# Kernel tuning notes

Measured on AMD Instinct MI355X. Metric: run time of the kernel, lower is better.

The kernel has to match this reference:

```python
import jax, jax.numpy as jnp
import numpy as np

N, E, D_IN, H, L, G = 50000, 800000, 128, 64, 3, 256
EPS_BN = 1e-5


def setup_inputs() -> dict:
    key = jax.random.key(0)
    ks = jax.random.split(key, 8)
    x = jax.random.normal(ks[0], (N, D_IN), dtype=jnp.float32)
    edge_index = jax.random.randint(ks[1], (2, E), 0, N)
    batch = jnp.sort(jax.random.randint(ks[2], (N,), 0, G))
    dims = [D_IN] + [H] * L
    params = {}
    for l in range(L):
        params[f"W{l}"] = jax.random.normal(ks[3 + l], (dims[l], H), jnp.float32) * (1.0 / np.sqrt(dims[l]))
        params[f"b{l}"] = jnp.zeros((H,), jnp.float32)
        params[f"gamma{l}"] = jnp.ones((H,), jnp.float32)
        params[f"beta{l}"] = jnp.zeros((H,), jnp.float32)
    return {"x": x, "edge_index": edge_index, "batch": batch, **params}


def _gcn_forward(x, edge_index, batch, Ws, bs, gammas, betas):
    n = x.shape[0]
    loop = jnp.arange(n)
    # GCNConv adds self-loops, then symmetric D^{-1/2} (A+I) D^{-1/2} normalization
    src = jnp.concatenate([edge_index[0], loop])
    dst = jnp.concatenate([edge_index[1], loop])
    deg = jax.ops.segment_sum(jnp.ones_like(src, jnp.float32), dst, num_segments=n)
    dinv = jax.lax.rsqrt(jnp.maximum(deg, 1.0))  # deg >= 1 thanks to self-loops
    norm = dinv[src] * dinv[dst]  # [E+N]

    zs = []
    z = x
    for W, b, g, be in zip(Ws, bs, gammas, betas):
        h = z @ W  # transform first, then aggregate (PyG GCNConv)
        agg = jax.ops.segment_sum(h[src] * norm[:, None], dst, num_segments=n) + b
        z = jax.nn.relu(agg)
        mu = z.mean(axis=0)
        var = z.var(axis=0)  # biased, as in BatchNorm training mode
        z = (z - mu) * jax.lax.rsqrt(var + EPS_BN) * g + be
        zs.append(z)

    cnt = jnp.maximum(
        jax.ops.segment_sum(jnp.ones((n,), jnp.float32), batch, num_segments=G), 1.0
    )
    gs = [jax.ops.segment_sum(z_, batch, num_segments=G) / cnt[:, None] for z_ in zs]

    zc = jnp.concatenate(zs, axis=1)  # [N, L*H]
    gc = jnp.concatenate(gs, axis=1)  # [G, L*H]

    def l2n(a):
        return a / jnp.maximum(jnp.linalg.norm(a, axis=1, keepdims=True), 1e-12)

    return l2n(zc), l2n(gc)


def reference(x, edge_index, batch, W0, b0, gamma0, beta0, W1, b1, gamma1, beta1, W2, b2, gamma2, beta2):
    return _gcn_forward(
        x, edge_index, batch,
        [W0, W1, W2], [b0, b1, b2],
        [gamma0, gamma1, gamma2], [beta0, beta1, beta2],
    )
```

## Files before the change

### kernel.cpp

```cpp
#include <hip/hip_runtime.h>
#include <hip/hip_fp16.h>
#include <cstdint>
#include <cstddef>

#define N_NODES 50000
#define N_EDGES 800000
#define DIM_IN 128
#define H_DIM 64
#define N_GRAPHS 256
#define EPS_BN 1e-5f
#define GEMM0_BLOCKS 782
#define CBLK 128
#define CHUNK 6250
#define HWORDS4 6250
#define SMEM_WORDS (DIM_IN * 64)

struct __align__(16) h8 { __half2 a, b, c, d; };
struct __align__(8)  h4 { __half2 a, b; };

__device__ inline void fma4(float4& a, float s, const float4& w) {
    a.x = fmaf(s, w.x, a.x);
    a.y = fmaf(s, w.y, a.y);
    a.z = fmaf(s, w.z, a.z);
    a.w = fmaf(s, w.w, a.w);
}

__device__ inline h4 pack_h4(float4 v) {
    h4 r;
    r.a = __float22half2_rn(make_float2(v.x, v.y));
    r.b = __float22half2_rn(make_float2(v.z, v.w));
    return r;
}


__global__ __launch_bounds__(256) void count_hist_k(const int* __restrict__ dst,
                                                    unsigned char* __restrict__ histG) {
    __shared__ unsigned int h[HWORDS4];
    for (int i = threadIdx.x; i < HWORDS4; i += 256) h[i] = 0;
    __syncthreads();
    int base = blockIdx.x * CHUNK;
    for (int i = threadIdx.x; i < CHUNK; i += 256) {
        int n = dst[base + i];
        atomicAdd(&h[n >> 3], 1u << (4 * (n & 7)));
    }
    __syncthreads();
    unsigned char* out = histG + (size_t)blockIdx.x * N_NODES;
    for (int n = threadIdx.x; n < N_NODES; n += 256)
        out[n] = (h[n >> 3] >> (4 * (n & 7))) & 0xF;
}

__global__ void blockscan_k(const unsigned char* __restrict__ histG,
                            unsigned char* __restrict__ baseG, int* __restrict__ counts) {
    int n = blockIdx.x * 256 + threadIdx.x;
    if (n >= N_NODES) return;
    int tot = 0;
    for (int b = 0; b < CBLK; b++) {
        unsigned char v = histG[(size_t)b * N_NODES + n];
        baseG[(size_t)b * N_NODES + n] = (unsigned char)tot;
        tot += v;
    }
    counts[n] = tot;
}

__global__ void scan_block_k(const int* __restrict__ counts, int* __restrict__ offsets,
                             int* __restrict__ blocksums) {
    __shared__ int sh[1024];
    int i = blockIdx.x * 1024 + threadIdx.x;
    int v = (i < N_NODES) ? counts[i] : 0;
    sh[threadIdx.x] = v;
    __syncthreads();
    for (int off = 1; off < 1024; off <<= 1) {
        int t = (threadIdx.x >= off) ? sh[threadIdx.x - off] : 0;
        __syncthreads();
        sh[threadIdx.x] += t;
        __syncthreads();
    }
    if (i < N_NODES) offsets[i] = sh[threadIdx.x] - v;
    if (threadIdx.x == 1023) blocksums[blockIdx.x] = sh[1023];
}

__global__ void scan_sums_k(int* blocksums, int nb) {
    if (threadIdx.x == 0 && blockIdx.x == 0) {
        int run = 0;
        for (int b = 0; b < nb; b++) { int t = blocksums[b]; blocksums[b] = run; run += t; }
    }
}

__global__ void finalize_offsets_k(int* __restrict__ offsets,
                                   const int* __restrict__ counts,
                                   const int* __restrict__ blocksums,
                                   float* __restrict__ dinv) {
    int i = blockIdx.x * blockDim.x + threadIdx.x;
    if (i >= N_NODES) return;
    offsets[i] = offsets[i] + blocksums[i >> 10];
    dinv[i] = rsqrtf((float)(counts[i] + 1));
}


__global__ __launch_bounds__(256) void gemm0_fill_k(
        const float* __restrict__ X, const float* __restrict__ W,
        const float* __restrict__ dinv, __half* __restrict__ hp,
        const int* __restrict__ src, const int* __restrict__ dst,
        const int* __restrict__ offsets, const unsigned char* __restrict__ baseG,
        unsigned short* __restrict__ ssrc) {
    __shared__ __align__(16) unsigned int smem[SMEM_WORDS];
    if (blockIdx.x < CBLK) {
        int b = blockIdx.x;
        for (int i = threadIdx.x; i < HWORDS4; i += 256) smem[i] = 0;
        __syncthreads();
        int base = b * CHUNK;
        const unsigned char* myBase = baseG + (size_t)b * N_NODES;
        for (int i = threadIdx.x; i < CHUNK; i += 256) {
            int n = dst[base + i];
            int s = src[base + i];
            unsigned int old = atomicAdd(&smem[n >> 3], 1u << (4 * (n & 7)));
            int rank = (old >> (4 * (n & 7))) & 0xF;
            ssrc[offsets[n] + myBase[n] + rank] = (unsigned short)s;
        }
        return;
    }
    int gb = blockIdx.x - CBLK;
    float* Wl = (float*)smem;
    for (int i = threadIdx.x * 4; i < DIM_IN * 64; i += 256 * 4)
        *(float4*)&Wl[i] = *(const float4*)&W[i];
    __syncthreads();
    int c4 = (threadIdx.x & 15) * 4;
    int n0 = gb * 64 + (threadIdx.x >> 4) * 4;
    if (n0 >= N_NODES) return;
    const float* zr = X + (size_t)n0 * DIM_IN;
    float4 acc0 = {0,0,0,0}, acc1 = {0,0,0,0}, acc2 = {0,0,0,0}, acc3 = {0,0,0,0};
    #pragma unroll 4
    for (int k = 0; k < DIM_IN; k += 4) {
        float4 w0 = *(float4*)&Wl[(k + 0) * 64 + c4];
        float4 w1 = *(float4*)&Wl[(k + 1) * 64 + c4];
        float4 w2 = *(float4*)&Wl[(k + 2) * 64 + c4];
        float4 w3 = *(float4*)&Wl[(k + 3) * 64 + c4];
        float4 z0 = *(const float4*)&zr[0 * DIM_IN + k];
        float4 z1 = *(const float4*)&zr[1 * DIM_IN + k];
        float4 z2 = *(const float4*)&zr[2 * DIM_IN + k];
        float4 z3 = *(const float4*)&zr[3 * DIM_IN + k];
        fma4(acc0, z0.x, w0); fma4(acc0, z0.y, w1); fma4(acc0, z0.z, w2); fma4(acc0, z0.w, w3);
        fma4(acc1, z1.x, w0); fma4(acc1, z1.y, w1); fma4(acc1, z1.z, w2); fma4(acc1, z1.w, w3);
        fma4(acc2, z2.x, w0); fma4(acc2, z2.y, w1); fma4(acc2, z2.z, w2); fma4(acc2, z2.w, w3);
        fma4(acc3, z3.x, w0); fma4(acc3, z3.y, w1); fma4(acc3, z3.z, w2); fma4(acc3, z3.w, w3);
    }
    float d0 = dinv[n0], d1 = dinv[n0 + 1], d2 = dinv[n0 + 2], d3 = dinv[n0 + 3];
    acc0.x *= d0; acc0.y *= d0; acc0.z *= d0; acc0.w *= d0;
    acc1.x *= d1; acc1.y *= d1; acc1.z *= d1; acc1.w *= d1;
    acc2.x *= d2; acc2.y *= d2; acc2.z *= d2; acc2.w *= d2;
    acc3.x *= d3; acc3.y *= d3; acc3.z *= d3; acc3.w *= d3;
    *(h4*)&hp[(size_t)(n0 + 0) * 64 + c4] = pack_h4(acc0);
    *(h4*)&hp[(size_t)(n0 + 1) * 64 + c4] = pack_h4(acc1);
    *(h4*)&hp[(size_t)(n0 + 2) * 64 + c4] = pack_h4(acc2);
    *(h4*)&hp[(size_t)(n0 + 3) * 64 + c4] = pack_h4(acc3);
}


__global__ __launch_bounds__(256) void gemm_h_k(
        const __half* __restrict__ Z, const float* __restrict__ W,
        const float* __restrict__ scale, const float* __restrict__ shift,
        const float* __restrict__ dinv, __half* __restrict__ hp) {
    __shared__ float Wl[H_DIM * 64];
    __shared__ float scl[64], shl[64];
    for (int i = threadIdx.x * 4; i < H_DIM * 64; i += 256 * 4)
        *(float4*)&Wl[i] = *(const float4*)&W[i];
    if (threadIdx.x < 64) { scl[threadIdx.x] = scale[threadIdx.x]; shl[threadIdx.x] = shift[threadIdx.x]; }
    __syncthreads();
    int c4 = (threadIdx.x & 15) * 4;
    int n0 = blockIdx.x * 64 + (threadIdx.x >> 4) * 4;
    if (n0 >= N_NODES) return;
    float4 acc0 = {0,0,0,0}, acc1 = {0,0,0,0}, acc2 = {0,0,0,0}, acc3 = {0,0,0,0};
    #pragma unroll 4
    for (int k = 0; k < H_DIM; k += 4) {
        float4 w0 = *(float4*)&Wl[(k + 0) * 64 + c4];
        float4 w1 = *(float4*)&Wl[(k + 1) * 64 + c4];
        float4 w2 = *(float4*)&Wl[(k + 2) * 64 + c4];
        float4 w3 = *(float4*)&Wl[(k + 3) * 64 + c4];
        float4 s4 = *(float4*)&scl[k];
        float4 f4 = *(float4*)&shl[k];
        #define DO_NODE(ACC, I)                                                        \
        {   h4 r = *(const h4*)&Z[(size_t)(n0 + I) * 64 + k];                          \
            float2 p = __half22float2(r.a), q = __half22float2(r.b);                   \
            float z0 = fmaf(p.x, s4.x, f4.x), z1 = fmaf(p.y, s4.y, f4.y);              \
            float z2 = fmaf(q.x, s4.z, f4.z), z3 = fmaf(q.y, s4.w, f4.w);              \
            fma4(ACC, z0, w0); fma4(ACC, z1, w1); fma4(ACC, z2, w2); fma4(ACC, z3, w3); }
        DO_NODE(acc0, 0) DO_NODE(acc1, 1) DO_NODE(acc2, 2) DO_NODE(acc3, 3)
        #undef DO_NODE
    }
    float d0 = dinv[n0], d1 = dinv[n0 + 1], d2 = dinv[n0 + 2], d3 = dinv[n0 + 3];
    acc0.x *= d0; acc0.y *= d0; acc0.z *= d0; acc0.w *= d0;
    acc1.x *= d1; acc1.y *= d1; acc1.z *= d1; acc1.w *= d1;
    acc2.x *= d2; acc2.y *= d2; acc2.z *= d2; acc2.w *= d2;
    acc3.x *= d3; acc3.y *= d3; acc3.z *= d3; acc3.w *= d3;
    *(h4*)&hp[(size_t)(n0 + 0) * 64 + c4] = pack_h4(acc0);
    *(h4*)&hp[(size_t)(n0 + 1) * 64 + c4] = pack_h4(acc1);
    *(h4*)&hp[(size_t)(n0 + 2) * 64 + c4] = pack_h4(acc2);
    *(h4*)&hp[(size_t)(n0 + 3) * 64 + c4] = pack_h4(acc3);
}


__global__ __launch_bounds__(256) void aggregate_k(
        const __half* __restrict__ hp, const float* __restrict__ dinv,
        const int* __restrict__ offsets, const int* __restrict__ counts,
        const unsigned short* __restrict__ ssrc, const float* __restrict__ bias,
        __half* __restrict__ zb) {
    int wid = (blockIdx.x * blockDim.x + threadIdx.x) >> 6;
    int lane = threadIdx.x & 63;
    int g = lane >> 3;
    int c8 = (lane & 7) * 8;
    float a0=0,a1=0,a2=0,a3=0,a4=0,a5=0,a6=0,a7=0;
    int s0 = offsets[wid];
    int ce = counts[wid];
    int e = g;
    for (; e + 8 < ce; e += 16) {
        int s1 = ssrc[s0 + e];
        int s2 = ssrc[s0 + e + 8];
        h8 v1 = *(const h8*)(hp + (size_t)s1 * 64 + c8);
        h8 v2 = *(const h8*)(hp + (size_t)s2 * 64 + c8);
        float2 f0 = __half22float2(v1.a), f1 = __half22float2(v1.b);
        float2 f2 = __half22float2(v1.c), f3 = __half22float2(v1.d);
        float2 g0 = __half22float2(v2.a), g1 = __half22float2(v2.b);
        float2 g2 = __half22float2(v2.c), g3 = __half22float2(v2.d);
        a0 += f0.x + g0.x; a1 += f0.y + g0.y; a2 += f1.x + g1.x; a3 += f1.y + g1.y;
        a4 += f2.x + g2.x; a5 += f2.y + g2.y; a6 += f3.x + g3.x; a7 += f3.y + g3.y;
    }
    if (e < ce) {
        int s = ssrc[s0 + e];
        h8 v = *(const h8*)(hp + (size_t)s * 64 + c8);
        float2 f0 = __half22float2(v.a), f1 = __half22float2(v.b);
        float2 f2 = __half22float2(v.c), f3 = __half22float2(v.d);
        a0 += f0.x; a1 += f0.y; a2 += f1.x; a3 += f1.y;
        a4 += f2.x; a5 += f2.y; a6 += f3.x; a7 += f3.y;
    }
    #define RED(A) A += __shfl_xor(A, 8); A += __shfl_xor(A, 16); A += __shfl_xor(A, 32);
    RED(a0) RED(a1) RED(a2) RED(a3) RED(a4) RED(a5) RED(a6) RED(a7)
    #undef RED
    if (g == 0) {
        h8 sv = *(const h8*)(hp + (size_t)wid * 64 + c8);
        float2 f0 = __half22float2(sv.a), f1 = __half22float2(sv.b);
        float2 f2 = __half22float2(sv.c), f3 = __half22float2(sv.d);
        float di = dinv[wid];
        float4 b0 = *(const float4*)&bias[c8];
        float4 b1 = *(const float4*)&bias[c8 + 4];
        float o0 = fmaxf(fmaf(a0 + f0.x, di, b0.x), 0.f);
        float o1 = fmaxf(fmaf(a1 + f0.y, di, b0.y), 0.f);
        float o2 = fmaxf(fmaf(a2 + f1.x, di, b0.z), 0.f);
        float o3 = fmaxf(fmaf(a3 + f1.y, di, b0.w), 0.f);
        float o4 = fmaxf(fmaf(a4 + f2.x, di, b1.x), 0.f);
        float o5 = fmaxf(fmaf(a5 + f2.y, di, b1.y), 0.f);
        float o6 = fmaxf(fmaf(a6 + f3.x, di, b1.z), 0.f);
        float o7 = fmaxf(fmaf(a7 + f3.y, di, b1.w), 0.f);
        h8 ov;
        ov.a = __float22half2_rn(make_float2(o0, o1));
        ov.b = __float22half2_rn(make_float2(o2, o3));
        ov.c = __float22half2_rn(make_float2(o4, o5));
        ov.d = __float22half2_rn(make_float2(o6, o7));
        *(h8*)(zb + (size_t)wid * 64 + c8) = ov;
    }
}


__global__ __launch_bounds__(256) void bn_stats_k(const __half* __restrict__ zb,
                                                  float* __restrict__ slots) {
    int slot = threadIdx.x & 7;
    int rp = threadIdx.x >> 3;
    float s[8], q[8];
    #pragma unroll
    for (int j = 0; j < 8; j++) { s[j] = 0.f; q[j] = 0.f; }
    for (int n = blockIdx.x * 32 + rp; n < N_NODES; n += 256 * 32) {
        h8 v = *(const h8*)(zb + (size_t)n * 64 + slot * 8);
        float2 f0 = __half22float2(v.a), f1 = __half22float2(v.b);
        float2 f2 = __half22float2(v.c), f3 = __half22float2(v.d);
        float x0 = f0.x, x1 = f0.y, x2 = f1.x, x3 = f1.y;
        float x4 = f2.x, x5 = f2.y, x6 = f3.x, x7 = f3.y;
        s[0] += x0; q[0] += x0 * x0; s[1] += x1; q[1] += x1 * x1;
        s[2] += x2; q[2] += x2 * x2; s[3] += x3; q[3] += x3 * x3;
        s[4] += x4; q[4] += x4 * x4; s[5] += x5; q[5] += x5 * x5;
        s[6] += x6; q[6] += x6 * x6; s[7] += x7; q[7] += x7 * x7;
    }
    #pragma unroll
    for (int j = 0; j < 8; j++) {
        float a = s[j];
        a += __shfl_xor(a, 8); a += __shfl_xor(a, 16); a += __shfl_xor(a, 32);
        s[j] = a;
        float b = q[j];
        b += __shfl_xor(b, 8); b += __shfl_xor(b, 16); b += __shfl_xor(b, 32);
        q[j] = b;
    }
    __shared__ float rs[4][64], rq[4][64];
    int w = threadIdx.x >> 6;
    if ((threadIdx.x & 63) < 8) {
        #pragma unroll
        for (int j = 0; j < 8; j++) {
            rs[w][slot * 8 + j] = s[j];
            rq[w][slot * 8 + j] = q[j];
        }
    }
    __syncthreads();
    int t = threadIdx.x;
    int rep = (blockIdx.x & 7) * 128;
    if (t < 64)
        atomicAdd(&slots[rep + t], rs[0][t] + rs[1][t] + rs[2][t] + rs[3][t]);
    else if (t < 128) {
        int c = t - 64;
        atomicAdd(&slots[rep + t], rq[0][c] + rq[1][c] + rq[2][c] + rq[3][c]);
    }
}

__global__ void bn_finalize_k(float* __restrict__ slots,
                              const float* __restrict__ gamma, const float* __restrict__ beta,
                              float* __restrict__ scale, float* __restrict__ shift) {
    __shared__ float red[128];
    int c = threadIdx.x;
    float v = 0.f;
    #pragma unroll
    for (int r = 0; r < 8; r++) v += slots[r * 128 + c];
    red[c] = v;
    __syncthreads();
    if (c < 64) {
        float mu = red[c] * (1.0f / N_NODES);
        float var = red[c + 64] * (1.0f / N_NODES) - mu * mu;
        float k = gamma[c] * rsqrtf(var + EPS_BN);
        scale[c] = k;
        shift[c] = beta[c] - mu * k;
    }
    #pragma unroll
    for (int i = 0; i < 8; i++) slots[i * 128 + c] = 0.f;
}


__global__ __launch_bounds__(256) void pool_k(
        const __half* __restrict__ zb0, const __half* __restrict__ zb1,
        const __half* __restrict__ zb2,
        const float* __restrict__ scaleAll, const float* __restrict__ shiftAll,
        const int* __restrict__ batch, float* __restrict__ gc) {
    int g = blockIdx.x;
    int lo = 0, hi = N_NODES;
    while (lo < hi) { int mid = (lo + hi) >> 1; if (batch[mid] < g) lo = mid + 1; else hi = mid; }
    int start = lo;
    hi = N_NODES;
    while (lo < hi) { int mid = (lo + hi) >> 1; if (batch[mid] < g + 1) lo = mid + 1; else hi = mid; }
    int end = lo;

    int slot = threadIdx.x & 7;
    int r = threadIdx.x >> 3;
    const __half* zbs[3] = {zb0, zb1, zb2};
    float acc[3][8];
    #pragma unroll
    for (int l = 0; l < 3; l++)
        #pragma unroll
        for (int j = 0; j < 8; j++) acc[l][j] = 0.f;
    #pragma unroll
    for (int l = 0; l < 3; l++) {
        const __half* z = zbs[l];
        for (int n = start + r; n < end; n += 32) {
            h8 v = *(const h8*)(z + (size_t)n * 64 + slot * 8);
            float2 f0 = __half22float2(v.a), f1 = __half22float2(v.b);
            float2 f2 = __half22float2(v.c), f3 = __half22float2(v.d);
            acc[l][0] += f0.x; acc[l][1] += f0.y; acc[l][2] += f1.x; acc[l][3] += f1.y;
            acc[l][4] += f2.x; acc[l][5] += f2.y; acc[l][6] += f3.x; acc[l][7] += f3.y;
        }
    }
    #pragma unroll
    for (int l = 0; l < 3; l++)
        #pragma unroll
        for (int j = 0; j < 8; j++) {
            float a = acc[l][j];
            a += __shfl_xor(a, 8);
            a += __shfl_xor(a, 16);
            a += __shfl_xor(a, 32);
            acc[l][j] = a;
        }
    __shared__ float red[4][3][64];
    int w = threadIdx.x >> 6;
    if ((threadIdx.x & 63) < 8) {
        #pragma unroll
        for (int l = 0; l < 3; l++)
            #pragma unroll
            for (int j = 0; j < 8; j++)
                red[w][l][slot * 8 + j] = acc[l][j];
    }
    __syncthreads();
    __shared__ float part[4];
    int t = threadIdx.x;
    float m = 0.f;
    if (t < 192) {
        int l = t >> 6, ch = t & 63;
        float s = red[0][l][ch] + red[1][l][ch] + red[2][l][ch] + red[3][l][ch];
        m = (end > start) ? fmaf(scaleAll[t], s / (float)(end - start), shiftAll[t]) : 0.f;
    }
    float q = m * m;
    #pragma unroll
    for (int off = 32; off; off >>= 1) q += __shfl_xor(q, off);
    if ((t & 63) == 0) part[t >> 6] = q;
    __syncthreads();
    float inv = 1.0f / fmaxf(sqrtf(part[0] + part[1] + part[2] + part[3]), 1e-12f);
    if (t < 192) gc[(size_t)g * 192 + t] = m * inv;
}

__global__ __launch_bounds__(256) void l2norm_zc_k(
        const __half* __restrict__ zb0, const __half* __restrict__ zb1,
        const __half* __restrict__ zb2,
        const float* __restrict__ scaleAll, const float* __restrict__ shiftAll,
        float* __restrict__ zc) {
    int wid = (blockIdx.x * blockDim.x + threadIdx.x) >> 6;
    int lane = threadIdx.x & 63;
    float a = fmaf(__half2float(zb0[(size_t)wid * 64 + lane]), scaleAll[lane],       shiftAll[lane]);
    float b = fmaf(__half2float(zb1[(size_t)wid * 64 + lane]), scaleAll[64 + lane],  shiftAll[64 + lane]);
    float c = fmaf(__half2float(zb2[(size_t)wid * 64 + lane]), scaleAll[128 + lane], shiftAll[128 + lane]);
    float s = a * a + b * b + c * c;
    #pragma unroll
    for (int off = 32; off; off >>= 1) s += __shfl_xor(s, off);
    float inv = 1.0f / fmaxf(sqrtf(s), 1e-12f);
    float* row = zc + (size_t)wid * 192;
    row[lane] = a * inv; row[lane + 64] = b * inv; row[lane + 128] = c * inv;
}


extern "C" void kernel_launch(void* const* d_in, const int* in_sizes, int n_in,
                              void* d_out, int out_size, void* d_ws, size_t ws_size,
                              hipStream_t stream) {
    const float* x     = (const float*)d_in[0];
    const int*   ei    = (const int*)d_in[1];
    const int*   batch = (const int*)d_in[2];
    const float* W[3]     = {(const float*)d_in[3],  (const float*)d_in[7],  (const float*)d_in[11]};
    const float* bias[3]  = {(const float*)d_in[4],  (const float*)d_in[8],  (const float*)d_in[12]};
    const float* gamma[3] = {(const float*)d_in[5],  (const float*)d_in[9],  (const float*)d_in[13]};
    const float* beta[3]  = {(const float*)d_in[6],  (const float*)d_in[10], (const float*)d_in[14]};
    const int* src = ei;
    const int* dst = ei + N_EDGES;

    float* out = (float*)d_out;
    float* zc = out;
    float* gc = out + (size_t)N_NODES * 192;

    char* w = (char*)d_ws;
    auto alloc = [&](size_t bytes) -> void* {
        void* p = (void*)w;
        w += (bytes + 255) / 256 * 256;
        return p;
    };
    int*            counts    = (int*)alloc(N_NODES * 4);
    int*            offsets   = (int*)alloc(N_NODES * 4);
    int*            blocksums = (int*)alloc(64 * 4);
    float*          dinv      = (float*)alloc(N_NODES * 4);
    unsigned short* ssrc      = (unsigned short*)alloc(N_EDGES * 2);
    __half*         hp        = (__half*)alloc((size_t)N_NODES * 64 * 2);
    __half*         zb[3];
    zb[0] = (__half*)alloc((size_t)N_NODES * 64 * 2);
    zb[1] = (__half*)alloc((size_t)N_NODES * 64 * 2);
    zb[2] = (__half*)alloc((size_t)N_NODES * 64 * 2);
    float*          slots     = (float*)alloc(8 * 128 * 4);
    float*          scaleAll  = (float*)alloc(192 * 4);
    float*          shiftAll  = (float*)alloc(192 * 4);
    unsigned char* histG = (unsigned char*)zb[1];
    unsigned char* baseG = (unsigned char*)zb[2];

    const int nscan = (N_NODES + 1023) / 1024;

    hipMemsetAsync(slots, 0, 8 * 128 * 4, stream);
    count_hist_k<<<CBLK, 256, 0, stream>>>(dst, histG);
    blockscan_k<<<(N_NODES + 255) / 256, 256, 0, stream>>>(histG, baseG, counts);
    scan_block_k<<<nscan, 1024, 0, stream>>>(counts, offsets, blocksums);
    scan_sums_k<<<1, 64, 0, stream>>>(blocksums, nscan);
    finalize_offsets_k<<<(N_NODES + 255) / 256, 256, 0, stream>>>(offsets, counts, blocksums, dinv);

    gemm0_fill_k<<<CBLK + GEMM0_BLOCKS, 256, 0, stream>>>(x, W[0], dinv, hp,
                                                          src, dst, offsets, baseG, ssrc);

    const int aggBlocks = N_NODES / 4;

    for (int l = 0; l < 3; l++) {
        if (l > 0)
            gemm_h_k<<<GEMM0_BLOCKS, 256, 0, stream>>>(zb[l - 1], W[l],
                                                       scaleAll + (l - 1) * 64, shiftAll + (l - 1) * 64,
                                                       dinv, hp);
        aggregate_k<<<aggBlocks, 256, 0, stream>>>(hp, dinv, offsets, counts, ssrc,
                                                   bias[l], zb[l]);
        bn_stats_k<<<256, 256, 0, stream>>>(zb[l], slots);
        bn_finalize_k<<<1, 128, 0, stream>>>(slots, gamma[l], beta[l],
                                             scaleAll + l * 64, shiftAll + l * 64);
    }

    pool_k<<<N_GRAPHS, 256, 0, stream>>>(zb[0], zb[1], zb[2], scaleAll, shiftAll, batch, gc);
    l2norm_zc_k<<<N_NODES / 4, 256, 0, stream>>>(zb[0], zb[1], zb[2], scaleAll, shiftAll, zc);
}
```

Baseline: 225.7 us.

## Replace per-node histogram CSR build with two-level bucketed counting sort

Result: faster. 204.7 us (-9.3%).

```diff
diff --git a/kernel.cpp b/kernel.cpp
--- a/kernel.cpp
+++ b/kernel.cpp
@@ -10,9 +10,11 @@
 #define N_GRAPHS 256
 #define EPS_BN 1e-5f
 #define GEMM0_BLOCKS 782
-#define CBLK 128
+#define NC 128
 #define CHUNK 6250
-#define HWORDS4 6250
+#define NB 256
+#define BUCKET_NODES 196
+#define LSS_CAP 4096
 #define SMEM_WORDS (DIM_IN * 64)
 
 struct __align__(16) h8 { __half2 a, b, c, d; };
@@ -33,93 +35,25 @@
 }
 
 
-__global__ __launch_bounds__(256) void count_hist_k(const int* __restrict__ dst,
-                                                    unsigned char* __restrict__ histG) {
-    __shared__ unsigned int h[HWORDS4];
-    for (int i = threadIdx.x; i < HWORDS4; i += 256) h[i] = 0;
-    __syncthreads();
-    int base = blockIdx.x * CHUNK;
-    for (int i = threadIdx.x; i < CHUNK; i += 256) {
-        int n = dst[base + i];
-        atomicAdd(&h[n >> 3], 1u << (4 * (n & 7)));
-    }
-    __syncthreads();
-    unsigned char* out = histG + (size_t)blockIdx.x * N_NODES;
-    for (int n = threadIdx.x; n < N_NODES; n += 256)
-        out[n] = (h[n >> 3] >> (4 * (n & 7))) & 0xF;
-}
-
-__global__ void blockscan_k(const unsigned char* __restrict__ histG,
-                            unsigned char* __restrict__ baseG, int* __restrict__ counts) {
-    int n = blockIdx.x * 256 + threadIdx.x;
-    if (n >= N_NODES) return;
-    int tot = 0;
-    for (int b = 0; b < CBLK; b++) {
-        unsigned char v = histG[(size_t)b * N_NODES + n];
-        baseG[(size_t)b * N_NODES + n] = (unsigned char)tot;
-        tot += v;
-    }
-    counts[n] = tot;
-}
-
-__global__ void scan_block_k(const int* __restrict__ counts, int* __restrict__ offsets,
-                             int* __restrict__ blocksums) {
-    __shared__ int sh[1024];
-    int i = blockIdx.x * 1024 + threadIdx.x;
-    int v = (i < N_NODES) ? counts[i] : 0;
-    sh[threadIdx.x] = v;
-    __syncthreads();
-    for (int off = 1; off < 1024; off <<= 1) {
-        int t = (threadIdx.x >= off) ? sh[threadIdx.x - off] : 0;
+__global__ __launch_bounds__(256) void cnt_gemm0_k(
+        const float* __restrict__ X, const float* __restrict__ W,
+        __half* __restrict__ hp, const int* __restrict__ dst,
+        int* __restrict__ cntM) {
+    __shared__ __align__(16) unsigned int smem[SMEM_WORDS];
+    if (blockIdx.x < NC) {
+        int* cl = (int*)smem;
+        if (threadIdx.x < NB) cl[threadIdx.x] = 0;
         __syncthreads();
-        sh[threadIdx.x] += t;
-        __syncthreads();
-    }
-    if (i < N_NODES) offsets[i] = sh[threadIdx.x] - v;
-    if (threadIdx.x == 1023) blocksums[blockIdx.x] = sh[1023];
-}
-
-__global__ void scan_sums_k(int* blocksums, int nb) {
-    if (threadIdx.x == 0 && blockIdx.x == 0) {
-        int run = 0;
-        for (int b = 0; b < nb; b++) { int t = blocksums[b]; blocksums[b] = run; run += t; }
-    }
-}
-
-__global__ void finalize_offsets_k(int* __restrict__ offsets,
-                                   const int* __restrict__ counts,
-                                   const int* __restrict__ blocksums,
-                                   float* __restrict__ dinv) {
-    int i = blockIdx.x * blockDim.x + threadIdx.x;
-    if (i >= N_NODES) return;
-    offsets[i] = offsets[i] + blocksums[i >> 10];
-    dinv[i] = rsqrtf((float)(counts[i] + 1));
-}
-
-
-__global__ __launch_bounds__(256) void gemm0_fill_k(
-        const float* __restrict__ X, const float* __restrict__ W,
-        const float* __restrict__ dinv, __half* __restrict__ hp,
-        const int* __restrict__ src, const int* __restrict__ dst,
-        const int* __restrict__ offsets, const unsigned char* __restrict__ baseG,
-        unsigned short* __restrict__ ssrc) {
-    __shared__ __align__(16) unsigned int smem[SMEM_WORDS];
-    if (blockIdx.x < CBLK) {
-        int b = blockIdx.x;
-        for (int i = threadIdx.x; i < HWORDS4; i += 256) smem[i] = 0;
-        __syncthreads();
-        int base = b * CHUNK;
-        const unsigned char* myBase = baseG + (size_t)b * N_NODES;
+        int base = blockIdx.x * CHUNK;
         for (int i = threadIdx.x; i < CHUNK; i += 256) {
             int n = dst[base + i];
-            int s = src[base + i];
-            unsigned int old = atomicAdd(&smem[n >> 3], 1u << (4 * (n & 7)));
-            int rank = (old >> (4 * (n & 7))) & 0xF;
-            ssrc[offsets[n] + myBase[n] + rank] = (unsigned short)s;
+            atomicAdd(&cl[n / BUCKET_NODES], 1);
         }
+        __syncthreads();
+        if (threadIdx.x < NB) cntM[blockIdx.x * NB + threadIdx.x] = cl[threadIdx.x];
         return;
     }
-    int gb = blockIdx.x - CBLK;
+    int gb = blockIdx.x - NC;
     float* Wl = (float*)smem;
     for (int i = threadIdx.x * 4; i < DIM_IN * 64; i += 256 * 4)
         *(float4*)&Wl[i] = *(const float4*)&W[i];
@@ -144,11 +78,6 @@
         fma4(acc2, z2.x, w0); fma4(acc2, z2.y, w1); fma4(acc2, z2.z, w2); fma4(acc2, z2.w, w3);
         fma4(acc3, z3.x, w0); fma4(acc3, z3.y, w1); fma4(acc3, z3.z, w2); fma4(acc3, z3.w, w3);
     }
-    float d0 = dinv[n0], d1 = dinv[n0 + 1], d2 = dinv[n0 + 2], d3 = dinv[n0 + 3];
-    acc0.x *= d0; acc0.y *= d0; acc0.z *= d0; acc0.w *= d0;
-    acc1.x *= d1; acc1.y *= d1; acc1.z *= d1; acc1.w *= d1;
-    acc2.x *= d2; acc2.y *= d2; acc2.z *= d2; acc2.w *= d2;
-    acc3.x *= d3; acc3.y *= d3; acc3.z *= d3; acc3.w *= d3;
     *(h4*)&hp[(size_t)(n0 + 0) * 64 + c4] = pack_h4(acc0);
     *(h4*)&hp[(size_t)(n0 + 1) * 64 + c4] = pack_h4(acc1);
     *(h4*)&hp[(size_t)(n0 + 2) * 64 + c4] = pack_h4(acc2);
@@ -156,10 +85,100 @@
 }
 
 
+__global__ void scanM_k(const int* __restrict__ cntM, int* __restrict__ baseM,
+                        int* __restrict__ beb) {
+    __shared__ int colsum[NB];
+    int w = threadIdx.x;
+    int tot = 0;
+    for (int c = 0; c < NC; c++) {
+        baseM[c * NB + w] = tot;
+        tot += cntM[c * NB + w];
+    }
+    colsum[w] = tot;
+    __syncthreads();
+    if (w == 0) {
+        int run = 0;
+        for (int b = 0; b < NB; b++) { beb[b] = run; run += colsum[b]; }
+        beb[NB] = run;
+    }
+}
+
+
+__global__ __launch_bounds__(256) void scatter_k(
+        const int* __restrict__ src, const int* __restrict__ dst,
+        const int* __restrict__ baseM, const int* __restrict__ beb,
+        unsigned int* __restrict__ ebuf) {
+    __shared__ int rk[NB];
+    int c = blockIdx.x;
+    if (threadIdx.x < NB) rk[threadIdx.x] = 0;
+    __syncthreads();
+    int base = c * CHUNK;
+    for (int i = threadIdx.x; i < CHUNK; i += 256) {
+        int n = dst[base + i];
+        int s = src[base + i];
+        int w = n / BUCKET_NODES;
+        int r = atomicAdd(&rk[w], 1);
+        ebuf[beb[w] + baseM[c * NB + w] + r] = ((unsigned)n << 16) | (unsigned)s;
+    }
+}
+
+
+__global__ __launch_bounds__(256) void fill_k(
+        const unsigned int* __restrict__ ebuf, const int* __restrict__ beb,
+        int* __restrict__ counts, int* __restrict__ offsets, float* __restrict__ dinv,
+        unsigned short* __restrict__ ssrc) {
+    int w = blockIdx.x;
+    int n0 = w * BUCKET_NODES;
+    int nn = min(BUCKET_NODES, N_NODES - n0);
+    int eb = beb[w];
+    int ec = beb[w + 1] - eb;
+    __shared__ int cnt[BUCKET_NODES];
+    __shared__ int sc[NB];
+    __shared__ unsigned short lssrc[LSS_CAP];
+    int t = threadIdx.x;
+    if (t < BUCKET_NODES) cnt[t] = 0;
+    __syncthreads();
+    for (int i = t; i < ec; i += 256) {
+        int nl = (int)(ebuf[eb + i] >> 16) - n0;
+        atomicAdd(&cnt[nl], 1);
+    }
+    __syncthreads();
+    int cj = (t < nn) ? cnt[t] : 0;
+    sc[t] = cj;
+    __syncthreads();
+    for (int off = 1; off < NB; off <<= 1) {
+        int a = (t >= off) ? sc[t - off] : 0;
+        __syncthreads();
+        sc[t] += a;
+        __syncthreads();
+    }
+    int offj = sc[t] - cj;
+    if (t < nn) {
+        int n = n0 + t;
+        counts[n] = cj;
+        offsets[n] = eb + offj;
+        dinv[n] = rsqrtf((float)(cj + 1));
+        cnt[t] = offj;
+    }
+    __syncthreads();
+    for (int i = t; i < ec; i += 256) {
+        unsigned int e = ebuf[eb + i];
+        int nl = (int)(e >> 16) - n0;
+        int p = atomicAdd(&cnt[nl], 1);
+        unsigned short s = (unsigned short)(e & 0xffffu);
+        if (p < LSS_CAP) lssrc[p] = s;
+        else ssrc[eb + p] = s;
+    }
+    __syncthreads();
+    int lim = min(ec, LSS_CAP);
+    for (int i = t; i < lim; i += 256) ssrc[eb + i] = lssrc[i];
+}
+
+
 __global__ __launch_bounds__(256) void gemm_h_k(
         const __half* __restrict__ Z, const float* __restrict__ W,
         const float* __restrict__ scale, const float* __restrict__ shift,
-        const float* __restrict__ dinv, __half* __restrict__ hp) {
+        __half* __restrict__ hp) {
     __shared__ float Wl[H_DIM * 64];
     __shared__ float scl[64], shl[64];
     for (int i = threadIdx.x * 4; i < H_DIM * 64; i += 256 * 4)
@@ -187,11 +206,6 @@
         DO_NODE(acc0, 0) DO_NODE(acc1, 1) DO_NODE(acc2, 2) DO_NODE(acc3, 3)
         #undef DO_NODE
     }
-    float d0 = dinv[n0], d1 = dinv[n0 + 1], d2 = dinv[n0 + 2], d3 = dinv[n0 + 3];
-    acc0.x *= d0; acc0.y *= d0; acc0.z *= d0; acc0.w *= d0;
-    acc1.x *= d1; acc1.y *= d1; acc1.z *= d1; acc1.w *= d1;
-    acc2.x *= d2; acc2.y *= d2; acc2.z *= d2; acc2.w *= d2;
-    acc3.x *= d3; acc3.y *= d3; acc3.z *= d3; acc3.w *= d3;
     *(h4*)&hp[(size_t)(n0 + 0) * 64 + c4] = pack_h4(acc0);
     *(h4*)&hp[(size_t)(n0 + 1) * 64 + c4] = pack_h4(acc1);
     *(h4*)&hp[(size_t)(n0 + 2) * 64 + c4] = pack_h4(acc2);
@@ -215,22 +229,32 @@
     for (; e + 8 < ce; e += 16) {
         int s1 = ssrc[s0 + e];
         int s2 = ssrc[s0 + e + 8];
+        float d1 = dinv[s1], d2 = dinv[s2];
         h8 v1 = *(const h8*)(hp + (size_t)s1 * 64 + c8);
         h8 v2 = *(const h8*)(hp + (size_t)s2 * 64 + c8);
         float2 f0 = __half22float2(v1.a), f1 = __half22float2(v1.b);
         float2 f2 = __half22float2(v1.c), f3 = __half22float2(v1.d);
         float2 g0 = __half22float2(v2.a), g1 = __half22float2(v2.b);
         float2 g2 = __half22float2(v2.c), g3 = __half22float2(v2.d);
-        a0 += f0.x + g0.x; a1 += f0.y + g0.y; a2 += f1.x + g1.x; a3 += f1.y + g1.y;
-        a4 += f2.x + g2.x; a5 += f2.y + g2.y; a6 += f3.x + g3.x; a7 += f3.y + g3.y;
+        a0 = fmaf(f0.x, d1, a0); a0 = fmaf(g0.x, d2, a0);
+        a1 = fmaf(f0.y, d1, a1); a1 = fmaf(g0.y, d2, a1);
+        a2 = fmaf(f1.x, d1, a2); a2 = fmaf(g1.x, d2, a2);
+        a3 = fmaf(f1.y, d1, a3); a3 = fmaf(g1.y, d2, a3);
+        a4 = fmaf(f2.x, d1, a4); a4 = fmaf(g2.x, d2, a4);
+        a5 = fmaf(f2.y, d1, a5); a5 = fmaf(g2.y, d2, a5);
+        a6 = fmaf(f3.x, d1, a6); a6 = fmaf(g3.x, d2, a6);
+        a7 = fmaf(f3.y, d1, a7); a7 = fmaf(g3.y, d2, a7);
     }
     if (e < ce) {
         int s = ssrc[s0 + e];
+        float d1 = dinv[s];
         h8 v = *(const h8*)(hp + (size_t)s * 64 + c8);
         float2 f0 = __half22float2(v.a), f1 = __half22float2(v.b);
         float2 f2 = __half22float2(v.c), f3 = __half22float2(v.d);
-        a0 += f0.x; a1 += f0.y; a2 += f1.x; a3 += f1.y;
-        a4 += f2.x; a5 += f2.y; a6 += f3.x; a7 += f3.y;
+        a0 = fmaf(f0.x, d1, a0); a1 = fmaf(f0.y, d1, a1);
+        a2 = fmaf(f1.x, d1, a2); a3 = fmaf(f1.y, d1, a3);
+        a4 = fmaf(f2.x, d1, a4); a5 = fmaf(f2.y, d1, a5);
+        a6 = fmaf(f3.x, d1, a6); a7 = fmaf(f3.y, d1, a7);
     }
     #define RED(A) A += __shfl_xor(A, 8); A += __shfl_xor(A, 16); A += __shfl_xor(A, 32);
     RED(a0) RED(a1) RED(a2) RED(a3) RED(a4) RED(a5) RED(a6) RED(a7)
@@ -242,14 +266,14 @@
         float di = dinv[wid];
         float4 b0 = *(const float4*)&bias[c8];
         float4 b1 = *(const float4*)&bias[c8 + 4];
-        float o0 = fmaxf(fmaf(a0 + f0.x, di, b0.x), 0.f);
-        float o1 = fmaxf(fmaf(a1 + f0.y, di, b0.y), 0.f);
-        float o2 = fmaxf(fmaf(a2 + f1.x, di, b0.z), 0.f);
-        float o3 = fmaxf(fmaf(a3 + f1.y, di, b0.w), 0.f);
-        float o4 = fmaxf(fmaf(a4 + f2.x, di, b1.x), 0.f);
-        float o5 = fmaxf(fmaf(a5 + f2.y, di, b1.y), 0.f);
-        float o6 = fmaxf(fmaf(a6 + f3.x, di, b1.z), 0.f);
-        float o7 = fmaxf(fmaf(a7 + f3.y, di, b1.w), 0.f);
+        float o0 = fmaxf(fmaf(fmaf(f0.x, di, a0), di, b0.x), 0.f);
+        float o1 = fmaxf(fmaf(fmaf(f0.y, di, a1), di, b0.y), 0.f);
+        float o2 = fmaxf(fmaf(fmaf(f1.x, di, a2), di, b0.z), 0.f);
+        float o3 = fmaxf(fmaf(fmaf(f1.y, di, a3), di, b0.w), 0.f);
+        float o4 = fmaxf(fmaf(fmaf(f2.x, di, a4), di, b1.x), 0.f);
+        float o5 = fmaxf(fmaf(fmaf(f2.y, di, a5), di, b1.y), 0.f);
+        float o6 = fmaxf(fmaf(fmaf(f3.x, di, a6), di, b1.z), 0.f);
+        float o7 = fmaxf(fmaf(fmaf(f3.y, di, a7), di, b1.w), 0.f);
         h8 ov;
         ov.a = __float22half2_rn(make_float2(o0, o1));
         ov.b = __float22half2_rn(make_float2(o2, o3));
@@ -442,7 +466,6 @@
     };
     int*            counts    = (int*)alloc(N_NODES * 4);
     int*            offsets   = (int*)alloc(N_NODES * 4);
-    int*            blocksums = (int*)alloc(64 * 4);
     float*          dinv      = (float*)alloc(N_NODES * 4);
     unsigned short* ssrc      = (unsigned short*)alloc(N_EDGES * 2);
     __half*         hp        = (__half*)alloc((size_t)N_NODES * 64 * 2);
@@ -453,20 +476,16 @@
     float*          slots     = (float*)alloc(8 * 128 * 4);
     float*          scaleAll  = (float*)alloc(192 * 4);
     float*          shiftAll  = (float*)alloc(192 * 4);
-    unsigned char* histG = (unsigned char*)zb[1];
-    unsigned char* baseG = (unsigned char*)zb[2];
-
-    const int nscan = (N_NODES + 1023) / 1024;
+    unsigned int* ebuf  = (unsigned int*)zb[1];
+    int*          cntM  = (int*)zb[2];
+    int*          baseM = (int*)((char*)zb[2] + NC * NB * 4);
+    int*          beb   = (int*)((char*)zb[2] + 2 * NC * NB * 4);
 
     hipMemsetAsync(slots, 0, 8 * 128 * 4, stream);
-    count_hist_k<<<CBLK, 256, 0, stream>>>(dst, histG);
-    blockscan_k<<<(N_NODES + 255) / 256, 256, 0, stream>>>(histG, baseG, counts);
-    scan_block_k<<<nscan, 1024, 0, stream>>>(counts, offsets, blocksums);
-    scan_sums_k<<<1, 64, 0, stream>>>(blocksums, nscan);
-    finalize_offsets_k<<<(N_NODES + 255) / 256, 256, 0, stream>>>(offsets, counts, blocksums, dinv);
-
-    gemm0_fill_k<<<CBLK + GEMM0_BLOCKS, 256, 0, stream>>>(x, W[0], dinv, hp,
-                                                          src, dst, offsets, baseG, ssrc);
+    cnt_gemm0_k<<<NC + GEMM0_BLOCKS, 256, 0, stream>>>(x, W[0], hp, dst, cntM);
+    scanM_k<<<1, NB, 0, stream>>>(cntM, baseM, beb);
+    scatter_k<<<NC, 256, 0, stream>>>(src, dst, baseM, beb, ebuf);
+    fill_k<<<NB, 256, 0, stream>>>(ebuf, beb, counts, offsets, dinv, ssrc);
 
     const int aggBlocks = N_NODES / 4;
 
@@ -474,7 +493,7 @@
         if (l > 0)
             gemm_h_k<<<GEMM0_BLOCKS, 256, 0, stream>>>(zb[l - 1], W[l],
                                                        scaleAll + (l - 1) * 64, shiftAll + (l - 1) * 64,
-                                                       dinv, hp);
+                                                       hp);
         aggregate_k<<<aggBlocks, 256, 0, stream>>>(hp, dinv, offsets, counts, ssrc,
                                                    bias[l], zb[l]);
         bn_stats_k<<<256, 256, 0, stream>>>(zb[l], slots);
```
